# Performance work log

Measured on AMD Instinct MI355X. Metric: run time of the kernel, lower is better.

Reference implementation:

```python
import jax, jax.numpy as jnp
from jax import lax
import numpy as np

B, T, U, V = 8, 256, 64, 512
BLANK_ID = 0


def setup_inputs() -> dict:
    key = jax.random.key(0)
    k1, k2, k3, k4 = jax.random.split(key, 4)
    pred_pad = jax.random.normal(k1, (B, T, U + 1, V), dtype=jnp.float32)
    target = jax.random.randint(k2, (B, U), 1, V, dtype=jnp.int32)
    pred_len = jax.random.randint(k3, (B,), T - 16, T + 1, dtype=jnp.int32)
    target_len = jax.random.randint(k4, (B,), U - 8, U + 1, dtype=jnp.int32)
    return {"pred_pad": pred_pad, "target": target,
            "pred_len": pred_len, "target_len": target_len}


def _rnnt_loss(log_probs, target, pred_len, target_len, blank_id):
    """Forward (alpha) DP of the RNN-T loss in the log semiring.

    log_probs: (B, T, U+1, V) log-softmax outputs of the joint network.
    Returns mean over batch of -log P(target | input).
    """
    b, t_max, u1, _ = log_probs.shape
    u_max = u1 - 1

    blank_lp = log_probs[..., blank_id]                    # (B, T, U+1)
    # emit_lp[b, t, u] = log p(target[b, u] | t, u) for u < U
    emit_lp = jnp.take_along_axis(
        log_probs[:, :, :u_max, :], target[:, None, :, None].astype(jnp.int32),
        axis=-1)[..., 0]                                   # (B, T, U)

    # alpha row at t = 0: only emissions along u.
    row0 = jnp.concatenate(
        [jnp.zeros((b, 1), log_probs.dtype),
         jnp.cumsum(emit_lp[:, 0, :], axis=-1)], axis=-1)  # (B, U+1)

    def time_step(prev_row, xs):
        blank_prev, emit_t = xs                            # (B,U+1), (B,U)
        a = prev_row + blank_prev                          # stay path (from t-1)

        def u_step(carry, xs_u):
            a_u, e_um1 = xs_u                              # (B,), (B,)
            new = jnp.logaddexp(a_u, carry + e_um1)
            return new, new

        init = a[:, 0]
        _, rest = lax.scan(u_step, init, (a[:, 1:].T, emit_t.T))  # (U, B)
        new_row = jnp.concatenate([init[:, None], rest.T], axis=-1)
        return new_row, new_row

    xs = (blank_lp[:, :-1, :].transpose(1, 0, 2),          # blank at t-1
          emit_lp[:, 1:, :].transpose(1, 0, 2))            # emit at t
    _, rows = lax.scan(time_step, row0, xs)                # (T-1, B, U+1)
    alpha = jnp.concatenate([row0[None], rows], axis=0)    # (T, B, U+1)

    b_idx = jnp.arange(b)
    t_last = pred_len - 1
    final_alpha = alpha[t_last, b_idx, target_len]
    final_blank = blank_lp[b_idx, t_last, target_len]
    return jnp.mean(-(final_alpha + final_blank))


def reference(pred_pad, target, pred_len, target_len):
    log_probs = jax.nn.log_softmax(pred_pad.astype(jnp.float32), axis=-1)
    return _rnnt_loss(log_probs, target, pred_len, target_len, BLANK_ID)
```

## Files before the change

kernel.cpp:

```cpp
#include <hip/hip_runtime.h>
#include <math.h>

#define BB 8
#define TT 256
#define UU 64
#define VV 512
#define U1 65
#define DD 328
#define W  80
#define BIG_NEG (-1e30f)

__device__ __forceinline__ float lae(float a, float b) {
    float mx = fmaxf(a, b);
    float mn = fminf(a, b);
    return mx + __logf(1.0f + __expf(mn - mx));
}

__global__ __launch_bounds__(256) void fill_kernel(float4* __restrict__ p, int n4) {
    int i = blockIdx.x * 256 + threadIdx.x;
    if (i < n4) p[i] = make_float4(BIG_NEG, BIG_NEG, BIG_NEG, BIG_NEG);
}

__global__ __launch_bounds__(256) void lse_kernel(
    const float* __restrict__ pred, const int* __restrict__ target,
    float* __restrict__ BL, float* __restrict__ EM)
{
    int u = blockIdx.x * 4 + (threadIdx.x >> 6);
    if (u > UU) return;
    int t = blockIdx.y, b = blockIdx.z;
    int lane = threadIdx.x & 63;
    const float* x = pred + ((size_t)((b * TT + t) * U1 + u)) * VV;
    float4 a = *(const float4*)(x + lane * 4);
    float4 c = *(const float4*)(x + 256 + lane * 4);

    float s = __expf(a.x) + __expf(a.y) + __expf(a.z) + __expf(a.w)
            + __expf(c.x) + __expf(c.y) + __expf(c.z) + __expf(c.w);
#pragma unroll
    for (int off = 1; off <= 32; off <<= 1) s += __shfl_xor(s, off, 64);
    float lse = __logf(s);

    int d = t + u + 1;
    float* BLr = BL + ((size_t)b * DD + d) * W;
    float* EMr = EM + ((size_t)b * DD + d) * W;
    if (lane == 0) BLr[u] = a.x - lse;
    if (u < UU) {
        int tgt = target[b * UU + u];
        int li = tgt >> 2, ci = tgt & 3;
        int owner = (li >= 64) ? li - 64 : li;
        if (lane == owner) {
            float4 v = (li >= 64) ? c : a;
            float xv = (ci == 0) ? v.x : (ci == 1) ? v.y : (ci == 2) ? v.z : v.w;
            EMr[u + 1] = xv - lse;
        }
    }
    if (u == 0 && t == 0 && lane == 1) EM[(size_t)b * DD * W] = 0.f;
}

__global__ __launch_bounds__(512) void dp_kernel(
    const float* __restrict__ BL, const float* __restrict__ EM,
    const int* __restrict__ pred_len, const int* __restrict__ target_len,
    float* __restrict__ out)
{
    int tid = threadIdx.x;
    int b = tid >> 6, l = tid & 63;
    const float* pB = BL + (size_t)b * DD * W;
    const float* pE = EM + (size_t)b * DD * W;
    int tlast = pred_len[b] - 1;
    int tlen  = target_len[b];
    int dmax  = tlast + tlen;

    float cur = 0.f, cur64 = 0.f;
    float blv[4], emv[4], b64[4], e64[4];
#pragma unroll
    for (int j = 0; j < 4; ++j) {
        blv[j] = pB[j * W + l];  emv[j] = pE[j * W + l];
        b64[j] = pB[j * W + 64]; e64[j] = pE[j * W + 64];
    }
    for (int d0 = 0; d0 <= dmax; d0 += 4) {
        float nb[4], ne[4], nb64[4], ne64[4];
#pragma unroll
        for (int j = 0; j < 4; ++j) {
            int r = d0 + 4 + j;
            nb[j]   = pB[r * W + l];  ne[j]   = pE[r * W + l];
            nb64[j] = pB[r * W + 64]; ne64[j] = pE[r * W + 64];
        }
#pragma unroll
        for (int j = 0; j < 4; ++j) {
            if (d0 + j <= dmax) {
                float old  = cur;
                float left = __shfl_up(cur, 1, 64);
                cur64 = lae(cur64 + b64[j], old + e64[j]);
                cur   = lae(old + blv[j], left + emv[j]);
            }
        }
#pragma unroll
        for (int j = 0; j < 4; ++j) { blv[j]=nb[j]; emv[j]=ne[j]; b64[j]=nb64[j]; e64[j]=ne64[j]; }
    }

    float v  = (tlen <= 63) ? __shfl(cur, tlen, 64) : __shfl(cur64, 63, 64);
    float fb = pB[(dmax + 1) * W + tlen];
    float loss_b = -(v + fb);

    __shared__ float part[BB];
    if (l == 0) part[b] = loss_b;
    __syncthreads();
    if (tid == 0) {
        float s = 0.f;
#pragma unroll
        for (int i = 0; i < BB; ++i) s += part[i];
        out[0] = s * (1.0f / BB);
    }
}

extern "C" void kernel_launch(void* const* d_in, const int* in_sizes, int n_in,
                              void* d_out, int out_size, void* d_ws, size_t ws_size,
                              hipStream_t stream)
{
    const float* pred       = (const float*)d_in[0];
    const int*   target     = (const int*)d_in[1];
    const int*   pred_len   = (const int*)d_in[2];
    const int*   target_len = (const int*)d_in[3];

    float* BL = (float*)d_ws;
    float* EM = BL + (size_t)BB * DD * W;

    int n4 = (2 * BB * DD * W) / 4;
    fill_kernel<<<(n4 + 255) / 256, 256, 0, stream>>>((float4*)d_ws, n4);
    lse_kernel<<<dim3(17, TT, BB), 256, 0, stream>>>(pred, target, BL, EM);
    dp_kernel<<<1, 512, 0, stream>>>(BL, EM, pred_len, target_len, (float*)d_out);
}
```

Baseline: 423.2 us.

## Use base-2 log domain, flatten LSE grid, fixed-length DP loop with bpermute

Switches the whole loss computation to base-2 log space using hardware exp2/log2 builtins, converting back with ln2 at the end. The LSE kernel uses a flat 1D grid over all rows, which removes the idle wavefronts of the old 17-block u tiling. The DP loop now runs a fixed 320 diagonals in chunks of 8 with deeper prefetch, using ds_bpermute for the neighbour shift. It captures the result at dmax instead of using per-step predicates, and runs the u=64 column only when tlen is 64. The cost is extra DP iterations past dmax and slight precision differences from the base conversion.

```diff
diff --git a/kernel.cpp b/kernel.cpp
--- a/kernel.cpp
+++ b/kernel.cpp
@@ -9,11 +9,24 @@
 #define DD 328
 #define W  80
 #define BIG_NEG (-1e30f)
+#define LOG2E 1.4426950408889634f
+#define LN2   0.6931471805599453f
 
-__device__ __forceinline__ float lae(float a, float b) {
+#if __has_builtin(__builtin_amdgcn_exp2f)
+#define FEXP2 __builtin_amdgcn_exp2f
+#else
+#define FEXP2 exp2f
+#endif
+#if __has_builtin(__builtin_amdgcn_logf)
+#define FLOG2 __builtin_amdgcn_logf
+#else
+#define FLOG2 __log2f
+#endif
+
+__device__ __forceinline__ float lae2(float a, float b) {
     float mx = fmaxf(a, b);
     float mn = fminf(a, b);
-    return mx + __logf(1.0f + __expf(mn - mx));
+    return mx + FLOG2(1.0f + FEXP2(mn - mx));
 }
 
 __global__ __launch_bounds__(256) void fill_kernel(float4* __restrict__ p, int n4) {
@@ -25,24 +38,28 @@
     const float* __restrict__ pred, const int* __restrict__ target,
     float* __restrict__ BL, float* __restrict__ EM)
 {
-    int u = blockIdx.x * 4 + (threadIdx.x >> 6);
-    if (u > UU) return;
-    int t = blockIdx.y, b = blockIdx.z;
+    int row  = blockIdx.x * 4 + (threadIdx.x >> 6);
     int lane = threadIdx.x & 63;
-    const float* x = pred + ((size_t)((b * TT + t) * U1 + u)) * VV;
+    const float* x = pred + (size_t)row * VV;
     float4 a = *(const float4*)(x + lane * 4);
     float4 c = *(const float4*)(x + 256 + lane * 4);
 
-    float s = __expf(a.x) + __expf(a.y) + __expf(a.z) + __expf(a.w)
-            + __expf(c.x) + __expf(c.y) + __expf(c.z) + __expf(c.w);
+    float s = FEXP2(a.x * LOG2E) + FEXP2(a.y * LOG2E)
+            + FEXP2(a.z * LOG2E) + FEXP2(a.w * LOG2E)
+            + FEXP2(c.x * LOG2E) + FEXP2(c.y * LOG2E)
+            + FEXP2(c.z * LOG2E) + FEXP2(c.w * LOG2E);
 #pragma unroll
     for (int off = 1; off <= 32; off <<= 1) s += __shfl_xor(s, off, 64);
-    float lse = __logf(s);
+    float lse2v = FLOG2(s);
 
-    int d = t + u + 1;
+    int u  = row % U1;
+    int bt = row / U1;
+    int b  = bt / TT;
+    int t  = bt % TT;
+    int d  = t + u + 1;
     float* BLr = BL + ((size_t)b * DD + d) * W;
     float* EMr = EM + ((size_t)b * DD + d) * W;
-    if (lane == 0) BLr[u] = a.x - lse;
+    if (lane == 0) BLr[u] = a.x * LOG2E - lse2v;
     if (u < UU) {
         int tgt = target[b * UU + u];
         int li = tgt >> 2, ci = tgt & 3;
@@ -50,10 +67,11 @@
         if (lane == owner) {
             float4 v = (li >= 64) ? c : a;
             float xv = (ci == 0) ? v.x : (ci == 1) ? v.y : (ci == 2) ? v.z : v.w;
-            EMr[u + 1] = xv - lse;
+            EMr[u + 1] = xv * LOG2E - lse2v;
         }
     }
-    if (u == 0 && t == 0 && lane == 1) EM[(size_t)b * DD * W] = 0.f;
+    if (u == 0 && t == 0 && lane == 1)
+        EM[(size_t)b * DD * W] = 0.f;
 }
 
 __global__ __launch_bounds__(512) void dp_kernel(
@@ -62,47 +80,74 @@
     float* __restrict__ out)
 {
     int tid = threadIdx.x;
-    int b = tid >> 6, l = tid & 63;
-    const float* pB = BL + (size_t)b * DD * W;
-    const float* pE = EM + (size_t)b * DD * W;
-    int tlast = pred_len[b] - 1;
-    int tlen  = target_len[b];
+    int l = tid & 63;
+    int bu = __builtin_amdgcn_readfirstlane(tid >> 6);
+    const float* pB = BL + (size_t)bu * DD * W;
+    const float* pE = EM + (size_t)bu * DD * W;
+    int tlast = pred_len[bu] - 1;
+    int tlen  = target_len[bu];
     int dmax  = tlast + tlen;
 
-    float cur = 0.f, cur64 = 0.f;
-    float blv[4], emv[4], b64[4], e64[4];
+    int baddr = ((l - 1) & 63) * 4;
+    float cur = 0.f, cur64 = 0.f, sv = 0.f, sv64 = 0.f;
+
+    float A[8], E[8];
 #pragma unroll
-    for (int j = 0; j < 4; ++j) {
-        blv[j] = pB[j * W + l];  emv[j] = pE[j * W + l];
-        b64[j] = pB[j * W + 64]; e64[j] = pE[j * W + 64];
-    }
-    for (int d0 = 0; d0 <= dmax; d0 += 4) {
-        float nb[4], ne[4], nb64[4], ne64[4];
+    for (int j = 0; j < 8; ++j) { A[j] = pB[j * W + l]; E[j] = pE[j * W + l]; }
+
+    if (tlen <= 63) {
+        for (int d0 = 0; d0 < 320; d0 += 8) {
+            float nA[8], nE[8];
 #pragma unroll
-        for (int j = 0; j < 4; ++j) {
-            int r = d0 + 4 + j;
-            nb[j]   = pB[r * W + l];  ne[j]   = pE[r * W + l];
-            nb64[j] = pB[r * W + 64]; ne64[j] = pE[r * W + 64];
+            for (int j = 0; j < 8; ++j) {
+                int r = d0 + 8 + j;
+                nA[j] = pB[r * W + l]; nE[j] = pE[r * W + l];
+            }
+#pragma unroll
+            for (int j = 0; j < 8; ++j) {
+                float old  = cur;
+                float left = __int_as_float(__builtin_amdgcn_ds_bpermute(
+                                  baddr, __float_as_int(cur)));
+                cur = lae2(old + A[j], left + E[j]);
+                if (d0 + j == dmax) sv = cur;
+            }
+#pragma unroll
+            for (int j = 0; j < 8; ++j) { A[j] = nA[j]; E[j] = nE[j]; }
         }
+    } else {
+        float A64[8], E64[8];
 #pragma unroll
-        for (int j = 0; j < 4; ++j) {
-            if (d0 + j <= dmax) {
+        for (int j = 0; j < 8; ++j) { A64[j] = pB[j * W + 64]; E64[j] = pE[j * W + 64]; }
+        for (int d0 = 0; d0 < 320; d0 += 8) {
+            float nA[8], nE[8], nA64[8], nE64[8];
+#pragma unroll
+            for (int j = 0; j < 8; ++j) {
+                int r = d0 + 8 + j;
+                nA[j]   = pB[r * W + l];  nE[j]   = pE[r * W + l];
+                nA64[j] = pB[r * W + 64]; nE64[j] = pE[r * W + 64];
+            }
+#pragma unroll
+            for (int j = 0; j < 8; ++j) {
                 float old  = cur;
-                float left = __shfl_up(cur, 1, 64);
-                cur64 = lae(cur64 + b64[j], old + e64[j]);
-                cur   = lae(old + blv[j], left + emv[j]);
+                float left = __int_as_float(__builtin_amdgcn_ds_bpermute(
+                                  baddr, __float_as_int(cur)));
+                cur64 = lae2(cur64 + A64[j], old + E64[j]);
+                cur   = lae2(old + A[j], left + E[j]);
+                if (d0 + j == dmax) { sv = cur; sv64 = cur64; }
+            }
+#pragma unroll
+            for (int j = 0; j < 8; ++j) {
+                A[j] = nA[j]; E[j] = nE[j]; A64[j] = nA64[j]; E64[j] = nE64[j];
             }
         }
-#pragma unroll
-        for (int j = 0; j < 4; ++j) { blv[j]=nb[j]; emv[j]=ne[j]; b64[j]=nb64[j]; e64[j]=ne64[j]; }
     }
 
-    float v  = (tlen <= 63) ? __shfl(cur, tlen, 64) : __shfl(cur64, 63, 64);
+    float v  = (tlen <= 63) ? __shfl(sv, tlen, 64) : __shfl(sv64, 63, 64);
     float fb = pB[(dmax + 1) * W + tlen];
-    float loss_b = -(v + fb);
+    float loss_b = -(v + fb) * LN2;
 
     __shared__ float part[BB];
-    if (l == 0) part[b] = loss_b;
+    if (l == 0) part[tid >> 6] = loss_b;
     __syncthreads();
     if (tid == 0) {
         float s = 0.f;
@@ -126,6 +171,7 @@
 
     int n4 = (2 * BB * DD * W) / 4;
     fill_kernel<<<(n4 + 255) / 256, 256, 0, stream>>>((float4*)d_ws, n4);
-    lse_kernel<<<dim3(17, TT, BB), 256, 0, stream>>>(pred, target, BL, EM);
+    int rows = BB * TT * U1;
+    lse_kernel<<<rows / 4, 256, 0, stream>>>(pred, target, BL, EM);
     dp_kernel<<<1, 512, 0, stream>>>(BL, EM, pred_len, target_len, (float*)d_out);
 }
```

Result: faster. 389.4 us (-8.0%).
